# Optimization experiments

Hardware: AMD Instinct MI355X
Metric: run time of the kernel (lower is better)

Reference implementation:

```python
import jax, jax.numpy as jnp
import numpy as np

C_IN, C_HID, N_HEADS = 128, 32, 4
INF = 1.0e9
LN_EPS = 1e-5


def setup_inputs() -> dict:
    key = jax.random.key(0)
    ks = jax.random.split(key, 12)
    B, I, J, C, H, D = 1, 384, 384, C_IN, N_HEADS, C_HID
    s = 0.02
    return {
        "x": jax.random.normal(ks[0], (B, I, J, C), dtype=jnp.float32),
        "mask": jnp.ones((B, I, J), dtype=jnp.float32),
        "ln_g": jnp.ones((C,), dtype=jnp.float32),
        "ln_b": jnp.zeros((C,), dtype=jnp.float32),
        "w_tri": jax.random.normal(ks[1], (C, H), dtype=jnp.float32) * s,
        "wq": jax.random.normal(ks[2], (C, H, D), dtype=jnp.float32) * s,
        "wk": jax.random.normal(ks[3], (C, H, D), dtype=jnp.float32) * s,
        "wv": jax.random.normal(ks[4], (C, H, D), dtype=jnp.float32) * s,
        "wg": jax.random.normal(ks[5], (C, H, D), dtype=jnp.float32) * s,
        "bg": jnp.ones((H, D), dtype=jnp.float32),
        "wo": jax.random.normal(ks[6], (H, D, C), dtype=jnp.float32) * s,
        "bo": jnp.zeros((C,), dtype=jnp.float32),
    }


def reference(x, mask, ln_g, ln_b, w_tri, wq, wk, wv, wg, bg, wo, bo):
    # LayerNorm over channel dim
    mu = jnp.mean(x, axis=-1, keepdims=True)
    var = jnp.mean(jnp.square(x - mu), axis=-1, keepdims=True)
    xn = (x - mu) * jax.lax.rsqrt(var + LN_EPS) * ln_g + ln_b  # [B,I,J,C]

    # mask bias: [B, I, 1, 1, J]
    mask_bias = (INF * (mask - 1.0))[..., :, None, None, :]
    # triangle bias: linear(x) -> [B,I,J,H] -> [B,1,H,I,J]
    tri_bias = jnp.einsum("bijc,ch->bhij", xn, w_tri)[:, None]

    scale = 1.0 / jnp.sqrt(jnp.asarray(C_HID, dtype=xn.dtype))
    # per-row attention over J: tensors [B, I, H, J, D]
    q = jnp.einsum("bixc,chd->bihxd", xn, wq) * scale
    k = jnp.einsum("bixc,chd->bihxd", xn, wk)
    v = jnp.einsum("bixc,chd->bihxd", xn, wv)

    logits = jnp.einsum("bihqd,bihkd->bihqk", q, k) + mask_bias + tri_bias
    a = jax.nn.softmax(logits, axis=-1)
    o = jnp.einsum("bihqk,bihkd->bihqd", a, v)  # [B,I,H,J,D]

    g = jax.nn.sigmoid(jnp.einsum("bixc,chd->bihxd", xn, wg) + bg[None, None, :, None, :])
    o = o * g
    out = jnp.einsum("bihxd,hdc->bixc", o, wo) + bo  # [B,I,J,C]
    return out
```

## Files before the change

kernel.cpp:

```cpp
#include <hip/hip_runtime.h>
#include <math.h>


#define I_DIM 384
#define J_DIM 384
#define C_DIM 128
#define H_DIM 4
#define D_DIM 32
#define NPOS (I_DIM * J_DIM)
#define Q_SCALE 0.17677669529663687f

typedef __attribute__((ext_vector_type(8))) short bf16x8;
typedef __attribute__((ext_vector_type(4))) float f32x4;

__device__ __forceinline__ float sigmoidf_(float v) {
    return 1.0f / (1.0f + __expf(-v));
}
__device__ __forceinline__ unsigned short f2bf(float f) {
    union { float f; unsigned u; } x; x.f = f;
    unsigned u = x.u;
    u += 0x7fffu + ((u >> 16) & 1u);
    return (unsigned short)(u >> 16);
}
__device__ __forceinline__ float bf2f(unsigned short v) {
    union { unsigned u; float f; } x; x.u = ((unsigned)v) << 16;
    return x.f;
}

__global__ __launch_bounds__(256) void prep_kernel(
    const float* __restrict__ wq, const float* __restrict__ wk,
    const float* __restrict__ wv, const float* __restrict__ wg,
    const float* __restrict__ wo, unsigned short* __restrict__ Wt)
{
    const int mat = blockIdx.x;
    const float* W = (mat == 0) ? wq : (mat == 1) ? wk : (mat == 2) ? wv
                    : (mat == 3) ? wg : wo;
    const float scale = (mat == 0) ? Q_SCALE : 1.0f;
    const int t = threadIdx.x;
    const int n = t >> 1, c0 = (t & 1) * 64;
#pragma unroll
    for (int u = 0; u < 8; ++u) {
        unsigned pk[4];
#pragma unroll
        for (int w = 0; w < 4; ++w) {
            const unsigned short a = f2bf(W[(size_t)(c0 + u * 8 + w * 2 + 0) * 128 + n] * scale);
            const unsigned short b = f2bf(W[(size_t)(c0 + u * 8 + w * 2 + 1) * 128 + n] * scale);
            pk[w] = (unsigned)a | ((unsigned)b << 16);
        }
        int4 q; q.x = pk[0]; q.y = pk[1]; q.z = pk[2]; q.w = pk[3];
        *(int4*)(Wt + (size_t)mat * 16384 + n * 128 + c0 + u * 8) = q;
    }
}

__global__ __launch_bounds__(256) void proj_kernel(
    const float* __restrict__ x, const float* __restrict__ ln_g,
    const float* __restrict__ ln_b, const float* __restrict__ w_tri,
    const unsigned short* __restrict__ Wt, const float* __restrict__ bg,
    unsigned short* __restrict__ qb, unsigned short* __restrict__ kb,
    unsigned short* __restrict__ vb, unsigned short* __restrict__ gb,
    float* __restrict__ tri)
{
    __shared__ unsigned short At[128 * 128];
    __shared__ unsigned short Bt[128 * 128];

    const int t = threadIdx.x;
    const int pos0 = blockIdx.x * 128;
    const int lane = t & 63, wave = t >> 6;
    const int q15 = lane & 15, quad = lane >> 4;

    {
        const int r = t >> 1, half = t & 1, c0 = half * 64;
        const float* xrow = x + (size_t)(pos0 + r) * C_DIM + c0;
        float xv[64];
        float s = 0.f, ss = 0.f;
#pragma unroll
        for (int u = 0; u < 16; ++u) {
            float4 v4 = ((const float4*)xrow)[u];
            xv[u * 4 + 0] = v4.x; xv[u * 4 + 1] = v4.y;
            xv[u * 4 + 2] = v4.z; xv[u * 4 + 3] = v4.w;
            s  += v4.x + v4.y + v4.z + v4.w;
            ss += v4.x * v4.x + v4.y * v4.y + v4.z * v4.z + v4.w * v4.w;
        }
        s  += __shfl_xor(s, 1);
        ss += __shfl_xor(ss, 1);
        const float mu  = s * (1.0f / 128.0f);
        const float var = ss * (1.0f / 128.0f) - mu * mu;
        const float rstd = rsqrtf(var + 1e-5f);

        float ptri[4] = {0.f, 0.f, 0.f, 0.f};
#pragma unroll
        for (int u = 0; u < 8; ++u) {
            const float4 g0 = ((const float4*)(ln_g + c0))[u * 2];
            const float4 g1 = ((const float4*)(ln_g + c0))[u * 2 + 1];
            const float4 b0 = ((const float4*)(ln_b + c0))[u * 2];
            const float4 b1 = ((const float4*)(ln_b + c0))[u * 2 + 1];
            float xn8[8];
            xn8[0] = (xv[u * 8 + 0] - mu) * rstd * g0.x + b0.x;
            xn8[1] = (xv[u * 8 + 1] - mu) * rstd * g0.y + b0.y;
            xn8[2] = (xv[u * 8 + 2] - mu) * rstd * g0.z + b0.z;
            xn8[3] = (xv[u * 8 + 3] - mu) * rstd * g0.w + b0.w;
            xn8[4] = (xv[u * 8 + 4] - mu) * rstd * g1.x + b1.x;
            xn8[5] = (xv[u * 8 + 5] - mu) * rstd * g1.y + b1.y;
            xn8[6] = (xv[u * 8 + 6] - mu) * rstd * g1.z + b1.z;
            xn8[7] = (xv[u * 8 + 7] - mu) * rstd * g1.w + b1.w;
#pragma unroll
            for (int w = 0; w < 8; ++w) {
                const float4 wt = ((const float4*)w_tri)[c0 + u * 8 + w];
                ptri[0] += xn8[w] * wt.x; ptri[1] += xn8[w] * wt.y;
                ptri[2] += xn8[w] * wt.z; ptri[3] += xn8[w] * wt.w;
            }
            unsigned pk[4];
#pragma unroll
            for (int w = 0; w < 4; ++w)
                pk[w] = (unsigned)f2bf(xn8[w * 2]) | ((unsigned)f2bf(xn8[w * 2 + 1]) << 16);
            int4 q4; q4.x = pk[0]; q4.y = pk[1]; q4.z = pk[2]; q4.w = pk[3];
            const int c = half * 8 + u;
            *(int4*)&At[r * 128 + ((c ^ (r & 7)) * 8)] = q4;
        }
#pragma unroll
        for (int hh = 0; hh < 4; ++hh) ptri[hh] += __shfl_xor(ptri[hh], 1);
        const int pos = pos0 + r;
        const int i = pos / J_DIM, j = pos - (pos / J_DIM) * J_DIM;
        const int h0 = half * 2;
        tri[((size_t)(h0 + 0) * J_DIM + j) * I_DIM + i] = ptri[h0 + 0];
        tri[((size_t)(h0 + 1) * J_DIM + j) * I_DIM + i] = ptri[h0 + 1];
    }

    const int m0 = wave * 32;
    for (int mat = 0; mat < 4; ++mat) {
        __syncthreads();
        {
            const int rn = t >> 1, half = t & 1;
            const unsigned short* src = Wt + (size_t)mat * 16384 + rn * 128 + half * 64;
#pragma unroll
            for (int u = 0; u < 8; ++u) {
                const int c = half * 8 + u;
                *(int4*)&Bt[rn * 128 + ((c ^ (rn & 7)) * 8)] = *(const int4*)(src + u * 8);
            }
        }
        __syncthreads();

        f32x4 acc[2][8];
#pragma unroll
        for (int mt = 0; mt < 2; ++mt)
#pragma unroll
            for (int nt = 0; nt < 8; ++nt) acc[mt][nt] = (f32x4){0.f, 0.f, 0.f, 0.f};

#pragma unroll
        for (int kk = 0; kk < 4; ++kk) {
            const int sw = ((kk * 4 + quad) ^ (q15 & 7)) * 8;
            const bf16x8 a0 = *(const bf16x8*)&At[(m0 + q15) * 128 + sw];
            const bf16x8 a1 = *(const bf16x8*)&At[(m0 + 16 + q15) * 128 + sw];
#pragma unroll
            for (int nt = 0; nt < 8; ++nt) {
                const bf16x8 b = *(const bf16x8*)&Bt[(nt * 16 + q15) * 128 + sw];
                acc[0][nt] = __builtin_amdgcn_mfma_f32_16x16x32_bf16(a0, b, acc[0][nt], 0, 0, 0);
                acc[1][nt] = __builtin_amdgcn_mfma_f32_16x16x32_bf16(a1, b, acc[1][nt], 0, 0, 0);
            }
        }

        __syncthreads();
#pragma unroll
        for (int mt = 0; mt < 2; ++mt)
#pragma unroll
            for (int nt = 0; nt < 8; ++nt) {
                const int col = nt * 16 + q15;
                const float bgl = (mat == 3) ? bg[col] : 0.f;
#pragma unroll
                for (int reg = 0; reg < 4; ++reg) {
                    float v = acc[mt][nt][reg];
                    if (mat == 3) v = sigmoidf_(v + bgl);
                    const int row = m0 + mt * 16 + quad * 4 + reg;
                    Bt[row * 128 + (((col >> 3) ^ (row & 7)) * 8) + (col & 7)] = f2bf(v);
                }
            }
        __syncthreads();
        {
            unsigned short* O = (mat == 0) ? qb : (mat == 1) ? kb : (mat == 2) ? vb : gb;
#pragma unroll
            for (int sgm = 0; sgm < 2; ++sgm) {
                const int ch = t + sgm * 256;
                const int r = ch >> 2, hh = ch & 3;
                const int pos = pos0 + r;
                const int i = pos / J_DIM, j = pos - (pos / J_DIM) * J_DIM;
                unsigned short* dst = O + (((size_t)i * H_DIM + hh) * J_DIM + j) * D_DIM;
#pragma unroll
                for (int w = 0; w < 4; ++w) {
                    const int c = hh * 4 + w;
                    *(int4*)(dst + w * 8) = *(const int4*)&Bt[r * 128 + ((c ^ (r & 7)) * 8)];
                }
            }
        }
    }
}

__global__ __launch_bounds__(256) void attn_kernel(
    const unsigned short* __restrict__ qb, const unsigned short* __restrict__ kb,
    const unsigned short* __restrict__ vb, unsigned short* gob,
    const float* __restrict__ triT, const float* __restrict__ mask)
{
    __shared__ unsigned short Klds[64 * 32];
    __shared__ unsigned short Vt[32 * 68];
    __shared__ unsigned short Plds[4][96 * 68];
    __shared__ float Mb[J_DIM];

    const int t = threadIdx.x;
    const int lane = t & 63, wave = t >> 6;
    const int q15 = lane & 15, quad = lane >> 4;
    const int i = blockIdx.x >> 2, h = blockIdx.x & 3;
    const size_t hb = (size_t)(i * H_DIM + h) * (J_DIM * D_DIM);
    const int m0 = wave * 96;

    for (int idx = t; idx < J_DIM; idx += 256)
        Mb[idx] = 1.0e9f * (mask[i * J_DIM + idx] - 1.0f);

    bf16x8 qf[6];
#pragma unroll
    for (int m = 0; m < 6; ++m)
        qf[m] = *(const bf16x8*)(qb + hb + (size_t)(m0 + m * 16 + q15) * D_DIM + quad * 8);

    f32x4 Oacc[6][2];
    float sums[6][4];
#pragma unroll
    for (int m = 0; m < 6; ++m) {
#pragma unroll
        for (int d2 = 0; d2 < 2; ++d2) Oacc[m][d2] = (f32x4){0.f, 0.f, 0.f, 0.f};
#pragma unroll
        for (int r = 0; r < 4; ++r) sums[m][r] = 0.f;
    }

    unsigned short* Pw = Plds[wave];
    const float* triH = triT + (size_t)h * J_DIM * I_DIM;

    for (int kt = 0; kt < 6; ++kt) {
        __syncthreads();
        {
            const int kp = t >> 2, du = (t & 3) * 8;
            const size_t gsrc = hb + (size_t)(kt * 64 + kp) * D_DIM + du;
            *(int4*)&Klds[kp * 32 + du] = *(const int4*)(kb + gsrc);
            int4 vv = *(const int4*)(vb + gsrc);
            const unsigned short* vs = (const unsigned short*)&vv;
#pragma unroll
            for (int u = 0; u < 8; ++u)
                Vt[(du + u) * 68 + kp] = vs[u];
        }
        __syncthreads();

#pragma unroll
        for (int nt = 0; nt < 4; ++nt) {
            const bf16x8 kf = *(const bf16x8*)&Klds[(nt * 16 + q15) * 32 + quad * 8];
            const float mb = Mb[kt * 64 + nt * 16 + q15];
            const float* tcol = triH + (size_t)(kt * 64 + nt * 16 + q15) * I_DIM;
#pragma unroll
            for (int m = 0; m < 6; ++m) {
                const float4 tb = *(const float4*)(tcol + m0 + m * 16 + quad * 4);
                f32x4 s = {0.f, 0.f, 0.f, 0.f};
                s = __builtin_amdgcn_mfma_f32_16x16x32_bf16(qf[m], kf, s, 0, 0, 0);
                const float p0 = __expf(s[0] + mb + tb.x);
                const float p1 = __expf(s[1] + mb + tb.y);
                const float p2 = __expf(s[2] + mb + tb.z);
                const float p3 = __expf(s[3] + mb + tb.w);
                sums[m][0] += p0; sums[m][1] += p1;
                sums[m][2] += p2; sums[m][3] += p3;
                const int row = m * 16 + quad * 4;
                const int col = nt * 16 + q15;
                Pw[(row + 0) * 68 + col] = f2bf(p0);
                Pw[(row + 1) * 68 + col] = f2bf(p1);
                Pw[(row + 2) * 68 + col] = f2bf(p2);
                Pw[(row + 3) * 68 + col] = f2bf(p3);
            }
        }

        bf16x8 vf[2][2];
#pragma unroll
        for (int ks = 0; ks < 2; ++ks)
#pragma unroll
            for (int d2 = 0; d2 < 2; ++d2)
                vf[ks][d2] = *(const bf16x8*)&Vt[(d2 * 16 + q15) * 68 + ks * 32 + quad * 8];
#pragma unroll
        for (int m = 0; m < 6; ++m) {
#pragma unroll
            for (int ks = 0; ks < 2; ++ks) {
                const bf16x8 af = *(const bf16x8*)&Pw[(m * 16 + q15) * 68 + ks * 32 + quad * 8];
                Oacc[m][0] = __builtin_amdgcn_mfma_f32_16x16x32_bf16(af, vf[ks][0], Oacc[m][0], 0, 0, 0);
                Oacc[m][1] = __builtin_amdgcn_mfma_f32_16x16x32_bf16(af, vf[ks][1], Oacc[m][1], 0, 0, 0);
            }
        }
    }

    float inv[6][4];
#pragma unroll
    for (int m = 0; m < 6; ++m)
#pragma unroll
        for (int r = 0; r < 4; ++r) {
            float s0 = sums[m][r];
            s0 += __shfl_xor(s0, 1); s0 += __shfl_xor(s0, 2);
            s0 += __shfl_xor(s0, 4); s0 += __shfl_xor(s0, 8);
            inv[m][r] = 1.0f / s0;
        }

#pragma unroll
    for (int m = 0; m < 6; ++m) {
        const int qrow = m0 + m * 16 + quad * 4;
#pragma unroll
        for (int d2 = 0; d2 < 2; ++d2) {
            const int d = d2 * 16 + q15;
#pragma unroll
            for (int r = 0; r < 4; ++r) {
                const size_t idx = hb + (size_t)(qrow + r) * D_DIM + d;
                const float g = bf2f(gob[idx]);
                gob[idx] = f2bf(Oacc[m][d2][r] * inv[m][r] * g);
            }
        }
    }
}

__global__ __launch_bounds__(256) void out_kernel(
    const unsigned short* __restrict__ og, const unsigned short* __restrict__ WtO,
    const float* __restrict__ bo, float* __restrict__ out)
{
    __shared__ unsigned short At[128 * 128];
    __shared__ unsigned short Bt[128 * 128];

    const int t = threadIdx.x;
    const int pos0 = blockIdx.x * 128;
    const int lane = t & 63, wave = t >> 6;
    const int q15 = lane & 15, quad = lane >> 4;

    {
        const int r = t >> 1, half = t & 1;
        const int pos = pos0 + r;
        const int i = pos / J_DIM, j = pos - (pos / J_DIM) * J_DIM;
#pragma unroll
        for (int u = 0; u < 8; ++u) {
            const int k0 = half * 64 + u * 8;
            const int hh = k0 >> 5, d0 = k0 & 31;
            const int4 v = *(const int4*)(og + (((size_t)i * H_DIM + hh) * J_DIM + j) * D_DIM + d0);
            const int c = half * 8 + u;
            *(int4*)&At[r * 128 + ((c ^ (r & 7)) * 8)] = v;
        }
        const unsigned short* src = WtO + r * 128 + half * 64;
#pragma unroll
        for (int u = 0; u < 8; ++u) {
            const int c = half * 8 + u;
            *(int4*)&Bt[r * 128 + ((c ^ (r & 7)) * 8)] = *(const int4*)(src + u * 8);
        }
    }
    __syncthreads();

    const int m0 = wave * 32;
    f32x4 acc[2][8];
#pragma unroll
    for (int mt = 0; mt < 2; ++mt)
#pragma unroll
        for (int nt = 0; nt < 8; ++nt) acc[mt][nt] = (f32x4){0.f, 0.f, 0.f, 0.f};

#pragma unroll
    for (int kk = 0; kk < 4; ++kk) {
        const int sw = ((kk * 4 + quad) ^ (q15 & 7)) * 8;
        const bf16x8 a0 = *(const bf16x8*)&At[(m0 + q15) * 128 + sw];
        const bf16x8 a1 = *(const bf16x8*)&At[(m0 + 16 + q15) * 128 + sw];
#pragma unroll
        for (int nt = 0; nt < 8; ++nt) {
            const bf16x8 b = *(const bf16x8*)&Bt[(nt * 16 + q15) * 128 + sw];
            acc[0][nt] = __builtin_amdgcn_mfma_f32_16x16x32_bf16(a0, b, acc[0][nt], 0, 0, 0);
            acc[1][nt] = __builtin_amdgcn_mfma_f32_16x16x32_bf16(a1, b, acc[1][nt], 0, 0, 0);
        }
    }

#pragma unroll
    for (int mt = 0; mt < 2; ++mt)
#pragma unroll
        for (int nt = 0; nt < 8; ++nt) {
            const float bov = bo[nt * 16 + q15];
#pragma unroll
            for (int reg = 0; reg < 4; ++reg) {
                const int pos = pos0 + m0 + mt * 16 + quad * 4 + reg;
                out[(size_t)pos * C_DIM + nt * 16 + q15] = acc[mt][nt][reg] + bov;
            }
        }
}

extern "C" void kernel_launch(void* const* d_in, const int* in_sizes, int n_in,
                              void* d_out, int out_size, void* d_ws, size_t ws_size,
                              hipStream_t stream)
{
    const float* x     = (const float*)d_in[0];
    const float* mask  = (const float*)d_in[1];
    const float* ln_g  = (const float*)d_in[2];
    const float* ln_b  = (const float*)d_in[3];
    const float* w_tri = (const float*)d_in[4];
    const float* wq    = (const float*)d_in[5];
    const float* wk    = (const float*)d_in[6];
    const float* wv    = (const float*)d_in[7];
    const float* wg    = (const float*)d_in[8];
    const float* bg    = (const float*)d_in[9];
    const float* wo    = (const float*)d_in[10];
    const float* bo    = (const float*)d_in[11];
    float* out = (float*)d_out;
    char* ws = (char*)d_ws;

    const size_t NE = (size_t)NPOS * 128;
    unsigned short* qb = (unsigned short*)ws;
    unsigned short* kb = (unsigned short*)(ws + NE * 2);
    unsigned short* vb = (unsigned short*)(ws + NE * 4);
    unsigned short* gb = (unsigned short*)(ws + NE * 6);
    float*         tri = (float*)(ws + NE * 8);
    unsigned short* Wt = (unsigned short*)(ws + NE * 8 + (size_t)NPOS * 4 * 4);

    prep_kernel<<<5, 256, 0, stream>>>(wq, wk, wv, wg, wo, Wt);
    proj_kernel<<<NPOS / 128, 256, 0, stream>>>(x, ln_g, ln_b, w_tri, Wt, bg,
                                                qb, kb, vb, gb, tri);
    attn_kernel<<<I_DIM * H_DIM, 256, 0, stream>>>(qb, kb, vb, gb, tri, mask);
    out_kernel<<<NPOS / 128, 256, 0, stream>>>(gb, Wt + 4 * 16384, bo, out);
}
```

Baseline: 522.5 us.

## Double-buffer K/V tiles and interleave per-row-block softmax with PV MFMAs

Double-buffers the K and V tiles in LDS. The next tile's global loads are issued into registers before computing the current tile, and the single pre-loop barrier pair becomes one barrier per iteration. The P staging buffer shrinks from a 96-row block per wave to two 16-row ping-pong slices, so each row block's PV MFMAs run right after its QK/exp work. This aims to hide global load latency and cut LDS footprint (possibly improving occupancy), at the cost of more live registers and a reordering that relies on intra-wave ordering of P writes and reads.

```diff
diff --git a/kernel.cpp b/kernel.cpp
--- a/kernel.cpp
+++ b/kernel.cpp
@@ -199,9 +199,9 @@
     const unsigned short* __restrict__ vb, unsigned short* gob,
     const float* __restrict__ triT, const float* __restrict__ mask)
 {
-    __shared__ unsigned short Klds[64 * 32];
-    __shared__ unsigned short Vt[32 * 68];
-    __shared__ unsigned short Plds[4][96 * 68];
+    __shared__ unsigned short Klds[2][64 * 32];
+    __shared__ unsigned short Vt[2][32 * 68];
+    __shared__ unsigned short Plds[4][2][16 * 68];
     __shared__ float Mb[J_DIM];
 
     const int t = threadIdx.x;
@@ -229,62 +229,82 @@
         for (int r = 0; r < 4; ++r) sums[m][r] = 0.f;
     }
 
-    unsigned short* Pw = Plds[wave];
     const float* triH = triT + (size_t)h * J_DIM * I_DIM;
 
+    const int kp = t >> 2, du = (t & 3) * 8;
+    int4 kreg, vreg;
+    {
+        const size_t gsrc = hb + (size_t)kp * D_DIM + du;
+        kreg = *(const int4*)(kb + gsrc);
+        vreg = *(const int4*)(vb + gsrc);
+        *(int4*)&Klds[0][kp * 32 + du] = kreg;
+        const unsigned short* vs = (const unsigned short*)&vreg;
+#pragma unroll
+        for (int u = 0; u < 8; ++u)
+            Vt[0][(du + u) * 68 + kp] = vs[u];
+    }
+    __syncthreads();
+
     for (int kt = 0; kt < 6; ++kt) {
-        __syncthreads();
-        {
-            const int kp = t >> 2, du = (t & 3) * 8;
-            const size_t gsrc = hb + (size_t)(kt * 64 + kp) * D_DIM + du;
-            *(int4*)&Klds[kp * 32 + du] = *(const int4*)(kb + gsrc);
-            int4 vv = *(const int4*)(vb + gsrc);
-            const unsigned short* vs = (const unsigned short*)&vv;
-#pragma unroll
-            for (int u = 0; u < 8; ++u)
-                Vt[(du + u) * 68 + kp] = vs[u];
-        }
-        __syncthreads();
-
-#pragma unroll
-        for (int nt = 0; nt < 4; ++nt) {
-            const bf16x8 kf = *(const bf16x8*)&Klds[(nt * 16 + q15) * 32 + quad * 8];
-            const float mb = Mb[kt * 64 + nt * 16 + q15];
-            const float* tcol = triH + (size_t)(kt * 64 + nt * 16 + q15) * I_DIM;
-#pragma unroll
-            for (int m = 0; m < 6; ++m) {
+        const int cur = kt & 1;
+
+        if (kt < 5) {
+            const size_t gsrc = hb + (size_t)((kt + 1) * 64 + kp) * D_DIM + du;
+            kreg = *(const int4*)(kb + gsrc);
+            vreg = *(const int4*)(vb + gsrc);
+        }
+
+        bf16x8 vf[2][2];
+#pragma unroll
+        for (int ks = 0; ks < 2; ++ks)
+#pragma unroll
+            for (int d2 = 0; d2 < 2; ++d2)
+                vf[ks][d2] = *(const bf16x8*)&Vt[cur][(d2 * 16 + q15) * 68 + ks * 32 + quad * 8];
+
+        float mbv[4];
+#pragma unroll
+        for (int nt = 0; nt < 4; ++nt)
+            mbv[nt] = Mb[kt * 64 + nt * 16 + q15];
+
+#pragma unroll
+        for (int m = 0; m < 6; ++m) {
+            unsigned short* Pw = &Plds[wave][m & 1][0];
+#pragma unroll
+            for (int nt = 0; nt < 4; ++nt) {
+                const bf16x8 kf = *(const bf16x8*)&Klds[cur][(nt * 16 + q15) * 32 + quad * 8];
+                const float* tcol = triH + (size_t)(kt * 64 + nt * 16 + q15) * I_DIM;
                 const float4 tb = *(const float4*)(tcol + m0 + m * 16 + quad * 4);
                 f32x4 s = {0.f, 0.f, 0.f, 0.f};
                 s = __builtin_amdgcn_mfma_f32_16x16x32_bf16(qf[m], kf, s, 0, 0, 0);
+                const float mb = mbv[nt];
                 const float p0 = __expf(s[0] + mb + tb.x);
                 const float p1 = __expf(s[1] + mb + tb.y);
                 const float p2 = __expf(s[2] + mb + tb.z);
                 const float p3 = __expf(s[3] + mb + tb.w);
                 sums[m][0] += p0; sums[m][1] += p1;
                 sums[m][2] += p2; sums[m][3] += p3;
-                const int row = m * 16 + quad * 4;
+                const int row = quad * 4;
                 const int col = nt * 16 + q15;
                 Pw[(row + 0) * 68 + col] = f2bf(p0);
                 Pw[(row + 1) * 68 + col] = f2bf(p1);
                 Pw[(row + 2) * 68 + col] = f2bf(p2);
                 Pw[(row + 3) * 68 + col] = f2bf(p3);
             }
-        }
-
-        bf16x8 vf[2][2];
-#pragma unroll
-        for (int ks = 0; ks < 2; ++ks)
-#pragma unroll
-            for (int d2 = 0; d2 < 2; ++d2)
-                vf[ks][d2] = *(const bf16x8*)&Vt[(d2 * 16 + q15) * 68 + ks * 32 + quad * 8];
-#pragma unroll
-        for (int m = 0; m < 6; ++m) {
 #pragma unroll
             for (int ks = 0; ks < 2; ++ks) {
-                const bf16x8 af = *(const bf16x8*)&Pw[(m * 16 + q15) * 68 + ks * 32 + quad * 8];
+                const bf16x8 af = *(const bf16x8*)&Pw[q15 * 68 + ks * 32 + quad * 8];
                 Oacc[m][0] = __builtin_amdgcn_mfma_f32_16x16x32_bf16(af, vf[ks][0], Oacc[m][0], 0, 0, 0);
                 Oacc[m][1] = __builtin_amdgcn_mfma_f32_16x16x32_bf16(af, vf[ks][1], Oacc[m][1], 0, 0, 0);
             }
+        }
+
+        if (kt < 5) {
+            *(int4*)&Klds[cur ^ 1][kp * 32 + du] = kreg;
+            const unsigned short* vs = (const unsigned short*)&vreg;
+#pragma unroll
+            for (int u = 0; u < 8; ++u)
+                Vt[cur ^ 1][(du + u) * 68 + kp] = vs[u];
+            __syncthreads();
         }
     }
 
```

Result: slower. 568.0 us (+8.7%).
